# Kernel tuning notes

Hardware: AMD Instinct MI355X
Metric: run time of the kernel (lower is better)

## Reference

```python
import jax, jax.numpy as jnp
import numpy as np
import math

# Hardcoded model constants (from source globals)
N_LAYERS = 4
MAX_SEQ_LEN = 34
VOCAB_SIZE = 14
TOK_DIM = 3
POS_DIM = 3
D_MODEL = 6
HEAD_DIM = 3
N_POS = 10
MAX_DIGITS = 10
ANSWER_LEN = 11
X_START, PLUS_POS, Y_START, EQ_POS, Z_START, EOS_POS = 0, 10, 11, 21, 22, 33
PLUS_TOKEN, EQUALS_TOKEN, EOS_TOKEN, PAD_TOKEN = 10, 11, 12, 13
BATCH = 16384


def _spiral(i, p):
    return (math.cos(2 * math.pi * i / p), math.sin(2 * math.pi * i / p), i / max(p - 1, 1))


def _build_pos_enc():
    pe = np.zeros((MAX_SEQ_LEN, POS_DIM), np.float32)
    for i in range(MAX_DIGITS):
        pe[X_START + i] = _spiral(i, N_POS)
    for i in range(MAX_DIGITS):
        pe[Y_START + i] = _spiral(i, N_POS)
    for i in range(min(ANSWER_LEN, N_POS)):
        pe[Z_START + i] = _spiral(i, N_POS)
    pe[Z_START + 10] = [0.0, 0.0, 1.5]
    pe[PLUS_POS] = [2.0, 0.0, -1.0]
    pe[EQ_POS] = [0.0, 2.0, -1.0]
    pe[EOS_POS] = [-2.0, 0.0, -1.0]
    return jnp.asarray(pe)


def _build_tok_emb():
    emb = np.zeros((VOCAB_SIZE, TOK_DIM), np.float32)
    for d in range(10):
        emb[d] = _spiral(d, 10)
    emb[PLUS_TOKEN] = [2.0, 0.0, -1.0]
    emb[EQUALS_TOKEN] = [0.0, 2.0, -1.0]
    emb[EOS_TOKEN] = [-2.0, 0.0, -1.0]
    emb[PAD_TOKEN] = [0.0, -2.0, -1.0]
    return jnp.asarray(emb)


def _xavier(key, shape):
    fan_out, fan_in = shape[-2], shape[-1]
    bound = math.sqrt(6.0 / (fan_in + fan_out))
    return jax.random.uniform(key, shape, jnp.float32, -bound, bound)


def setup_inputs() -> dict:
    key = jax.random.key(0)
    ks = jax.random.split(key, 10)
    L = N_LAYERS
    return {
        "idx": jax.random.randint(ks[0], (BATCH, MAX_SEQ_LEN), 0, VOCAB_SIZE),
        "tok_emb": _build_tok_emb(),
        "pos_enc": _build_pos_enc(),
        "ln_w": jnp.ones((L, D_MODEL), jnp.float32),
        "ln_b": jnp.zeros((L, D_MODEL), jnp.float32),
        "q1w": _xavier(ks[1], (L, HEAD_DIM, TOK_DIM)),
        "k1w": _xavier(ks[2], (L, HEAD_DIM, TOK_DIM)),
        "v1w": _xavier(ks[3], (L, HEAD_DIM, TOK_DIM)),
        "q2w": _xavier(ks[4], (L, HEAD_DIM, POS_DIM)),
        "k2w": _xavier(ks[5], (L, HEAD_DIM, POS_DIM)),
        "v2w": _xavier(ks[6], (L, HEAD_DIM, POS_DIM)),
        "out_w": _xavier(ks[7], (L, D_MODEL, 2 * HEAD_DIM)),
        "lnf_w": jnp.ones((D_MODEL,), jnp.float32),
        "lnf_b": jnp.zeros((D_MODEL,), jnp.float32),
        "head_w": _xavier(ks[8], (VOCAB_SIZE, D_MODEL)),
    }


def _layernorm(x, w, b, eps=1e-5):
    m = jnp.mean(x, -1, keepdims=True)
    v = jnp.mean(jnp.square(x - m), -1, keepdims=True)
    return (x - m) * jax.lax.rsqrt(v + eps) * w + b


def _attend(q, k, v, mask):
    # q,k,v: [B,T,HEAD_DIM]; mask: [T,T] bool lower-triangular
    s = jnp.einsum('bqd,bkd->bqk', q, k) / math.sqrt(HEAD_DIM)
    s = jnp.where(mask, s, jnp.finfo(s.dtype).min)
    return jnp.einsum('bqk,bkd->bqd', jax.nn.softmax(s, axis=-1), v)


def reference(idx, tok_emb, pos_enc, ln_w, ln_b, q1w, k1w, v1w, q2w, k2w, v2w, out_w, lnf_w, lnf_b, head_w):
    B, T = idx.shape
    tok = tok_emb[idx]                                   # [B,T,3]
    pos = jnp.broadcast_to(pos_enc[:T], (B, T, POS_DIM))  # [B,T,3]
    x = jnp.concatenate([tok, pos], axis=-1)             # [B,T,6]
    mask = jnp.tril(jnp.ones((T, T), bool))
    for l in range(N_LAYERS):
        h = _layernorm(x, ln_w[l], ln_b[l])
        ht, hp = h[..., :TOK_DIM], h[..., TOK_DIM:]
        o1 = _attend(ht @ q1w[l].T, ht @ k1w[l].T, ht @ v1w[l].T, mask)
        o2 = _attend(hp @ q2w[l].T, hp @ k2w[l].T, hp @ v2w[l].T, mask)
        x = x + jnp.concatenate([o1, o2], axis=-1) @ out_w[l].T
    x = _layernorm(x, lnf_w, lnf_b)
    return x @ head_w.T                                  # [B,T,VOCAB]
```

## Files before the change

### kernel.cpp

```cpp
#include <hip/hip_runtime.h>
#include <math.h>

#define N_LAYERS 4
#define SEQ      34
#define BATCH_N  16384
#define NE       16
#define NSLOT    8
#define NT       5
#define VOCAB    14
#define QSCALE   0.8329806647638704f

typedef float f32x2 __attribute__((ext_vector_type(2)));

static __device__ __forceinline__ f32x2 mk2(float a, float b) {
    f32x2 r; r.x = a; r.y = b; return r;
}

__global__ __launch_bounds__(128) void addtrans_kernel(
    const int*   __restrict__ idx,
    const float* __restrict__ tok_emb,
    const float* __restrict__ pos_enc,
    const float* __restrict__ ln_w,
    const float* __restrict__ ln_b,
    const float* __restrict__ q1w,
    const float* __restrict__ k1w,
    const float* __restrict__ v1w,
    const float* __restrict__ q2w,
    const float* __restrict__ k2w,
    const float* __restrict__ v2w,
    const float* __restrict__ out_w,
    const float* __restrict__ lnf_w,
    const float* __restrict__ lnf_b,
    const float* __restrict__ head_w,
    float* __restrict__ out)
{
    __shared__ float4 kvs[3 * SEQ + 1][NE];

    const int x = threadIdx.x & (NE - 1);
    const int y = threadIdx.x >> 4;
    const int b = (int)blockIdx.x * NE + x;

    int tp[NT];
    tp[0] = (y < 2) ? (32 + y) : (24 + y);
    tp[1] = y;
    tp[2] = 8 + y;
    tp[3] = 16 + y;
    tp[4] = (y < 2) ? (24 + y) : -1;
    const int jmax = tp[0];

    float xs[NT][6];
    #pragma unroll
    for (int k = 0; k < NT; ++k) {
        const int t = tp[k];
        if (t >= 0) {
            const int tok = idx[(size_t)b * SEQ + t];
            xs[k][0] = tok_emb[tok * 3 + 0];
            xs[k][1] = tok_emb[tok * 3 + 1];
            xs[k][2] = tok_emb[tok * 3 + 2];
            xs[k][3] = pos_enc[t * 3 + 0];
            xs[k][4] = pos_enc[t * 3 + 1];
            xs[k][5] = pos_enc[t * 3 + 2];
        }
    }

    f32x2 qp[NT][3];

    for (int l = 0; l < N_LAYERS; ++l) {
        __syncthreads();

        #pragma unroll
        for (int k = 0; k < NT; ++k) {
            const int t = tp[k];
            if (t >= 0) {
                float h[6];
                {
                    const float* v = xs[k];
                    float m = (v[0]+v[1]+v[2]+v[3]+v[4]+v[5]) * (1.0f/6.0f);
                    float var = 0.f;
                    #pragma unroll
                    for (int i = 0; i < 6; ++i) { float d = v[i]-m; var += d*d; }
                    var *= (1.0f/6.0f);
                    float r = rsqrtf(var + 1e-5f);
                    #pragma unroll
                    for (int i = 0; i < 6; ++i)
                        h[i] = (v[i]-m) * r * ln_w[l*6+i] + ln_b[l*6+i];
                }
                float kk[6], vv[6];
                #pragma unroll
                for (int i = 0; i < 3; ++i) {
                    const int w = l*9 + i*3;
                    float q1 = (q1w[w]*h[0] + q1w[w+1]*h[1] + q1w[w+2]*h[2]) * QSCALE;
                    float q2 = (q2w[w]*h[3] + q2w[w+1]*h[4] + q2w[w+2]*h[5]) * QSCALE;
                    qp[k][i] = mk2(q1, q2);
                    kk[i]    =  k1w[w]*h[0] + k1w[w+1]*h[1] + k1w[w+2]*h[2];
                    vv[i]    =  v1w[w]*h[0] + v1w[w+1]*h[1] + v1w[w+2]*h[2];
                    kk[3+i]  =  k2w[w]*h[3] + k2w[w+1]*h[4] + k2w[w+2]*h[5];
                    vv[3+i]  =  v2w[w]*h[3] + v2w[w+1]*h[4] + v2w[w+2]*h[5];
                }
                kvs[0*SEQ + t][x] = make_float4(kk[0], kk[3], kk[1], kk[4]);
                kvs[1*SEQ + t][x] = make_float4(kk[2], kk[5], vv[0], vv[3]);
                kvs[2*SEQ + t][x] = make_float4(vv[1], vv[4], vv[2], vv[5]);
            }
        }
        __syncthreads();

        f32x2 ls[NT], acc[NT][3];
        #pragma unroll
        for (int k = 0; k < NT; ++k) {
            ls[k] = mk2(0.f, 0.f);
            acc[k][0] = acc[k][1] = acc[k][2] = mk2(0.f, 0.f);
        }
        float4 c0 = kvs[0][x], c1 = kvs[SEQ][x], c2 = kvs[2*SEQ][x];
        #pragma unroll 2
        for (int j = 0; j <= jmax; ++j) {
            float4 n0 = kvs[j + 1][x];
            float4 n1 = kvs[SEQ + j + 1][x];
            float4 n2 = kvs[2*SEQ + j + 1][x];
            f32x2 kp0 = mk2(c0.x, c0.y), kp1 = mk2(c0.z, c0.w), kp2 = mk2(c1.x, c1.y);
            f32x2 vp0 = mk2(c1.z, c1.w), vp1 = mk2(c2.x, c2.y), vp2 = mk2(c2.z, c2.w);
            #pragma unroll
            for (int k = 0; k < NT; ++k) {
                if (k == 0 || j <= tp[k]) {
                    f32x2 s = qp[k][0]*kp0 + qp[k][1]*kp1 + qp[k][2]*kp2;
                    f32x2 p = mk2(__builtin_amdgcn_exp2f(s.x),
                                  __builtin_amdgcn_exp2f(s.y));
                    ls[k] += p;
                    acc[k][0] += p*vp0; acc[k][1] += p*vp1; acc[k][2] += p*vp2;
                }
            }
            c0 = n0; c1 = n1; c2 = n2;
        }

        #pragma unroll
        for (int k = 0; k < NT; ++k) {
            if (tp[k] >= 0) {
                const float i1 = __builtin_amdgcn_rcpf(ls[k].x);
                const float i2 = __builtin_amdgcn_rcpf(ls[k].y);
                float o[6] = { acc[k][0].x*i1, acc[k][1].x*i1, acc[k][2].x*i1,
                               acc[k][0].y*i2, acc[k][1].y*i2, acc[k][2].y*i2 };
                #pragma unroll
                for (int i = 0; i < 6; ++i) {
                    const int w = l*36 + i*6;
                    xs[k][i] += out_w[w+0]*o[0] + out_w[w+1]*o[1] + out_w[w+2]*o[2]
                              + out_w[w+3]*o[3] + out_w[w+4]*o[4] + out_w[w+5]*o[5];
                }
            }
        }
    }

    #pragma unroll
    for (int k = 0; k < NT; ++k) {
        const int t = tp[k];
        if (t >= 0) {
            float hf[6];
            {
                const float* v = xs[k];
                float m = (v[0]+v[1]+v[2]+v[3]+v[4]+v[5]) * (1.0f/6.0f);
                float var = 0.f;
                #pragma unroll
                for (int i = 0; i < 6; ++i) { float d = v[i]-m; var += d*d; }
                var *= (1.0f/6.0f);
                float r = rsqrtf(var + 1e-5f);
                #pragma unroll
                for (int i = 0; i < 6; ++i)
                    hf[i] = (v[i]-m) * r * lnf_w[i] + lnf_b[i];
            }
            float lg[VOCAB];
            #pragma unroll
            for (int c = 0; c < VOCAB; ++c) {
                const int w = c*6;
                lg[c] = head_w[w+0]*hf[0] + head_w[w+1]*hf[1] + head_w[w+2]*hf[2]
                      + head_w[w+3]*hf[3] + head_w[w+4]*hf[4] + head_w[w+5]*hf[5];
            }
            float2* op = (float2*)(out + ((size_t)b * SEQ + t) * VOCAB);
            #pragma unroll
            for (int c = 0; c < 7; ++c)
                op[c] = make_float2(lg[2*c], lg[2*c+1]);
        }
    }
}

extern "C" void kernel_launch(void* const* d_in, const int* in_sizes, int n_in,
                              void* d_out, int out_size, void* d_ws, size_t ws_size,
                              hipStream_t stream) {
    const int*   idx     = (const int*)  d_in[0];
    const float* tok_emb = (const float*)d_in[1];
    const float* pos_enc = (const float*)d_in[2];
    const float* ln_w    = (const float*)d_in[3];
    const float* ln_b    = (const float*)d_in[4];
    const float* q1w     = (const float*)d_in[5];
    const float* k1w     = (const float*)d_in[6];
    const float* v1w     = (const float*)d_in[7];
    const float* q2w     = (const float*)d_in[8];
    const float* k2w     = (const float*)d_in[9];
    const float* v2w     = (const float*)d_in[10];
    const float* out_w   = (const float*)d_in[11];
    const float* lnf_w   = (const float*)d_in[12];
    const float* lnf_b   = (const float*)d_in[13];
    const float* head_w  = (const float*)d_in[14];
    float* out = (float*)d_out;

    const int grid = BATCH_N / NE;
    addtrans_kernel<<<grid, NE * NSLOT, 0, stream>>>(
        idx, tok_emb, pos_enc, ln_w, ln_b,
        q1w, k1w, v1w, q2w, k2w, v2w,
        out_w, lnf_w, lnf_b, head_w, out);
}
```

Measured before the change: 139.4 us.

## Stage logits in shared memory for coalesced float4 stores and pack math into f32x2

The final logits are written into a shared-memory staging buffer laid out per block, then copied to global memory with fully coalesced float4 stores instead of strided per-thread float2 stores. The K/V shared layout becomes interleaved per position, [t][3][NE], instead of three separate planes. The Q/K/V projections, output projection and head matmul are rewritten with packed f32x2 arithmetic. This enlarges shared memory per block, which may lower occupancy, and adds an extra barrier and copy pass.

```diff
diff --git a/kernel.cpp b/kernel.cpp
--- a/kernel.cpp
+++ b/kernel.cpp
@@ -15,6 +15,8 @@
 static __device__ __forceinline__ f32x2 mk2(float a, float b) {
     f32x2 r; r.x = a; r.y = b; return r;
 }
+
+#define SM_BYTES (NE * SEQ * VOCAB * 4)
 
 __global__ __launch_bounds__(128) void addtrans_kernel(
     const int*   __restrict__ idx,
@@ -34,7 +36,8 @@
     const float* __restrict__ head_w,
     float* __restrict__ out)
 {
-    __shared__ float4 kvs[3 * SEQ + 1][NE];
+    __shared__ __align__(16) char smraw[SM_BYTES];
+    float4 (*kvs)[3][NE] = (float4 (*)[3][NE])smraw;
 
     const int x = threadIdx.x & (NE - 1);
     const int y = threadIdx.x >> 4;
@@ -85,21 +88,27 @@
                     for (int i = 0; i < 6; ++i)
                         h[i] = (v[i]-m) * r * ln_w[l*6+i] + ln_b[l*6+i];
                 }
-                float kk[6], vv[6];
+                f32x2 hp0 = mk2(h[0], h[3]);
+                f32x2 hp1 = mk2(h[1], h[4]);
+                f32x2 hp2 = mk2(h[2], h[5]);
+                f32x2 kkp[3], vvp[3];
                 #pragma unroll
                 for (int i = 0; i < 3; ++i) {
                     const int w = l*9 + i*3;
-                    float q1 = (q1w[w]*h[0] + q1w[w+1]*h[1] + q1w[w+2]*h[2]) * QSCALE;
-                    float q2 = (q2w[w]*h[3] + q2w[w+1]*h[4] + q2w[w+2]*h[5]) * QSCALE;
-                    qp[k][i] = mk2(q1, q2);
-                    kk[i]    =  k1w[w]*h[0] + k1w[w+1]*h[1] + k1w[w+2]*h[2];
-                    vv[i]    =  v1w[w]*h[0] + v1w[w+1]*h[1] + v1w[w+2]*h[2];
-                    kk[3+i]  =  k2w[w]*h[3] + k2w[w+1]*h[4] + k2w[w+2]*h[5];
-                    vv[3+i]  =  v2w[w]*h[3] + v2w[w+1]*h[4] + v2w[w+2]*h[5];
-                }
-                kvs[0*SEQ + t][x] = make_float4(kk[0], kk[3], kk[1], kk[4]);
-                kvs[1*SEQ + t][x] = make_float4(kk[2], kk[5], vv[0], vv[3]);
-                kvs[2*SEQ + t][x] = make_float4(vv[1], vv[4], vv[2], vv[5]);
+                    f32x2 q = mk2(q1w[w  ], q2w[w  ]) * hp0
+                            + mk2(q1w[w+1], q2w[w+1]) * hp1
+                            + mk2(q1w[w+2], q2w[w+2]) * hp2;
+                    qp[k][i] = q * QSCALE;
+                    kkp[i]   = mk2(k1w[w  ], k2w[w  ]) * hp0
+                             + mk2(k1w[w+1], k2w[w+1]) * hp1
+                             + mk2(k1w[w+2], k2w[w+2]) * hp2;
+                    vvp[i]   = mk2(v1w[w  ], v2w[w  ]) * hp0
+                             + mk2(v1w[w+1], v2w[w+1]) * hp1
+                             + mk2(v1w[w+2], v2w[w+2]) * hp2;
+                }
+                kvs[t][0][x] = make_float4(kkp[0].x, kkp[0].y, kkp[1].x, kkp[1].y);
+                kvs[t][1][x] = make_float4(kkp[2].x, kkp[2].y, vvp[0].x, vvp[0].y);
+                kvs[t][2][x] = make_float4(vvp[1].x, vvp[1].y, vvp[2].x, vvp[2].y);
             }
         }
         __syncthreads();
@@ -110,12 +119,14 @@
             ls[k] = mk2(0.f, 0.f);
             acc[k][0] = acc[k][1] = acc[k][2] = mk2(0.f, 0.f);
         }
-        float4 c0 = kvs[0][x], c1 = kvs[SEQ][x], c2 = kvs[2*SEQ][x];
+        const float4* r0 = &kvs[0][0][x];
+        float4 c0 = r0[0*NE], c1 = r0[1*NE], c2 = r0[2*NE];
         #pragma unroll 2
         for (int j = 0; j <= jmax; ++j) {
-            float4 n0 = kvs[j + 1][x];
-            float4 n1 = kvs[SEQ + j + 1][x];
-            float4 n2 = kvs[2*SEQ + j + 1][x];
+            const float4* rn = &kvs[j + 1][0][x];
+            float4 n0 = rn[0*NE];
+            float4 n1 = rn[1*NE];
+            float4 n2 = rn[2*NE];
             f32x2 kp0 = mk2(c0.x, c0.y), kp1 = mk2(c0.z, c0.w), kp2 = mk2(c1.x, c1.y);
             f32x2 vp0 = mk2(c1.z, c1.w), vp1 = mk2(c2.x, c2.y), vp2 = mk2(c2.z, c2.w);
             #pragma unroll
@@ -134,20 +145,25 @@
         #pragma unroll
         for (int k = 0; k < NT; ++k) {
             if (tp[k] >= 0) {
-                const float i1 = __builtin_amdgcn_rcpf(ls[k].x);
-                const float i2 = __builtin_amdgcn_rcpf(ls[k].y);
-                float o[6] = { acc[k][0].x*i1, acc[k][1].x*i1, acc[k][2].x*i1,
-                               acc[k][0].y*i2, acc[k][1].y*i2, acc[k][2].y*i2 };
+                const f32x2 inv = mk2(__builtin_amdgcn_rcpf(ls[k].x),
+                                      __builtin_amdgcn_rcpf(ls[k].y));
+                f32x2 op0 = acc[k][0] * inv;
+                f32x2 op1 = acc[k][1] * inv;
+                f32x2 op2 = acc[k][2] * inv;
                 #pragma unroll
                 for (int i = 0; i < 6; ++i) {
                     const int w = l*36 + i*6;
-                    xs[k][i] += out_w[w+0]*o[0] + out_w[w+1]*o[1] + out_w[w+2]*o[2]
-                              + out_w[w+3]*o[3] + out_w[w+4]*o[4] + out_w[w+5]*o[5];
-                }
-            }
-        }
-    }
-
+                    f32x2 t2 = mk2(out_w[w+0], out_w[w+3]) * op0
+                             + mk2(out_w[w+1], out_w[w+4]) * op1
+                             + mk2(out_w[w+2], out_w[w+5]) * op2;
+                    xs[k][i] += t2.x + t2.y;
+                }
+            }
+        }
+    }
+
+    __syncthreads();
+    f32x2* st2 = (f32x2*)smraw;
     #pragma unroll
     for (int k = 0; k < NT; ++k) {
         const int t = tp[k];
@@ -165,18 +181,27 @@
                 for (int i = 0; i < 6; ++i)
                     hf[i] = (v[i]-m) * r * lnf_w[i] + lnf_b[i];
             }
-            float lg[VOCAB];
             #pragma unroll
-            for (int c = 0; c < VOCAB; ++c) {
-                const int w = c*6;
-                lg[c] = head_w[w+0]*hf[0] + head_w[w+1]*hf[1] + head_w[w+2]*hf[2]
-                      + head_w[w+3]*hf[3] + head_w[w+4]*hf[4] + head_w[w+5]*hf[5];
-            }
-            float2* op = (float2*)(out + ((size_t)b * SEQ + t) * VOCAB);
-            #pragma unroll
-            for (int c = 0; c < 7; ++c)
-                op[c] = make_float2(lg[2*c], lg[2*c+1]);
-        }
+            for (int c = 0; c < 7; ++c) {
+                const int w0 = (2*c) * 6, w1 = (2*c + 1) * 6;
+                f32x2 lg = mk2(head_w[w0+0], head_w[w1+0]) * hf[0]
+                         + mk2(head_w[w0+1], head_w[w1+1]) * hf[1]
+                         + mk2(head_w[w0+2], head_w[w1+2]) * hf[2]
+                         + mk2(head_w[w0+3], head_w[w1+3]) * hf[3]
+                         + mk2(head_w[w0+4], head_w[w1+4]) * hf[4]
+                         + mk2(head_w[w0+5], head_w[w1+5]) * hf[5];
+                st2[x*238 + t*7 + c] = lg;
+            }
+        }
+    }
+    __syncthreads();
+
+    {
+        const float4* st4 = (const float4*)smraw;
+        float4* o4 = (float4*)(out + (size_t)blockIdx.x * (NE * SEQ * VOCAB));
+        #pragma unroll
+        for (int i = threadIdx.x; i < (NE * SEQ * VOCAB) / 4; i += NE * NSLOT)
+            o4[i] = st4[i];
     }
 }
 
```

Result: slower. 148.7 us (+6.7%).

## Assign contiguous query-row blocks per thread slot and specialize attention loop by row count

Applied to the files above, without the earlier changes.

Replaces the strided assignment of sequence positions to the 8 thread slots with contiguous runs of 5, 3 or 4 rows, chosen so causal-attention work is roughly balanced across slots. Because each slot's rows are adjacent, its key loop length (jmax) covers little wasted work for the lower rows. The attention loop is instantiated separately for 5-row and 4-row slots so the smaller variant uses fewer registers and skips the unused row. The cost is code duplication and the wave-level divergence between y<4 and y>=4 branches, although each wave of 64 threads holds 4 slots with the same y class.

```diff
diff --git a/kernel.cpp b/kernel.cpp
--- a/kernel.cpp
+++ b/kernel.cpp
@@ -40,12 +40,15 @@
     const int y = threadIdx.x >> 4;
     const int b = (int)blockIdx.x * NE + x;
 
+    int base, nrows;
+    if (y < 4) { base = 5 * y;                                nrows = 5; }
+    else { const int z = y - 4;
+           base  = (z < 2) ? (20 + 3 * z) : (26 + 4 * (z - 2));
+           nrows = (z < 2) ? 3 : 4; }
     int tp[NT];
-    tp[0] = (y < 2) ? (32 + y) : (24 + y);
-    tp[1] = y;
-    tp[2] = 8 + y;
-    tp[3] = 16 + y;
-    tp[4] = (y < 2) ? (24 + y) : -1;
+    #pragma unroll
+    for (int k = 0; k < NT; ++k)
+        tp[k] = (k < nrows) ? (base + nrows - 1 - k) : -1;
     const int jmax = tp[0];
 
     float xs[NT][6];
@@ -64,6 +67,51 @@
     }
 
     f32x2 qp[NT][3];
+
+    #define ATTN_EPI(NTK) \
+    { \
+        f32x2 ls[NTK], acc[NTK][3]; \
+        _Pragma("unroll") \
+        for (int k = 0; k < NTK; ++k) { \
+            ls[k] = mk2(0.f, 0.f); \
+            acc[k][0] = acc[k][1] = acc[k][2] = mk2(0.f, 0.f); \
+        } \
+        float4 c0 = kvs[0][x], c1 = kvs[SEQ][x], c2 = kvs[2*SEQ][x]; \
+        _Pragma("unroll 2") \
+        for (int j = 0; j <= jmax; ++j) { \
+            float4 n0 = kvs[j + 1][x]; \
+            float4 n1 = kvs[SEQ + j + 1][x]; \
+            float4 n2 = kvs[2*SEQ + j + 1][x]; \
+            f32x2 kp0 = mk2(c0.x, c0.y), kp1 = mk2(c0.z, c0.w), kp2 = mk2(c1.x, c1.y); \
+            f32x2 vp0 = mk2(c1.z, c1.w), vp1 = mk2(c2.x, c2.y), vp2 = mk2(c2.z, c2.w); \
+            _Pragma("unroll") \
+            for (int k = 0; k < NTK; ++k) { \
+                if (k == 0 || j <= tp[k]) {    \
+                    f32x2 s = qp[k][0]*kp0 + qp[k][1]*kp1 + qp[k][2]*kp2; \
+                    f32x2 p = mk2(__builtin_amdgcn_exp2f(s.x), \
+                                  __builtin_amdgcn_exp2f(s.y)); \
+                    ls[k] += p; \
+                    acc[k][0] += p*vp0; acc[k][1] += p*vp1; acc[k][2] += p*vp2; \
+                } \
+            } \
+            c0 = n0; c1 = n1; c2 = n2; \
+        } \
+        _Pragma("unroll") \
+        for (int k = 0; k < NTK; ++k) { \
+            if (tp[k] >= 0) { \
+                const float i1 = __builtin_amdgcn_rcpf(ls[k].x); \
+                const float i2 = __builtin_amdgcn_rcpf(ls[k].y); \
+                float o[6] = { acc[k][0].x*i1, acc[k][1].x*i1, acc[k][2].x*i1, \
+                               acc[k][0].y*i2, acc[k][1].y*i2, acc[k][2].y*i2 }; \
+                _Pragma("unroll") \
+                for (int i = 0; i < 6; ++i) { \
+                    const int w = l*36 + i*6; \
+                    xs[k][i] += out_w[w+0]*o[0] + out_w[w+1]*o[1] + out_w[w+2]*o[2] \
+                              + out_w[w+3]*o[3] + out_w[w+4]*o[4] + out_w[w+5]*o[5]; \
+                } \
+            } \
+        } \
+    }
 
     for (int l = 0; l < N_LAYERS; ++l) {
         __syncthreads();
@@ -104,49 +152,9 @@
         }
         __syncthreads();
 
-        f32x2 ls[NT], acc[NT][3];
-        #pragma unroll
-        for (int k = 0; k < NT; ++k) {
-            ls[k] = mk2(0.f, 0.f);
-            acc[k][0] = acc[k][1] = acc[k][2] = mk2(0.f, 0.f);
-        }
-        float4 c0 = kvs[0][x], c1 = kvs[SEQ][x], c2 = kvs[2*SEQ][x];
-        #pragma unroll 2
-        for (int j = 0; j <= jmax; ++j) {
-            float4 n0 = kvs[j + 1][x];
-            float4 n1 = kvs[SEQ + j + 1][x];
-            float4 n2 = kvs[2*SEQ + j + 1][x];
-            f32x2 kp0 = mk2(c0.x, c0.y), kp1 = mk2(c0.z, c0.w), kp2 = mk2(c1.x, c1.y);
-            f32x2 vp0 = mk2(c1.z, c1.w), vp1 = mk2(c2.x, c2.y), vp2 = mk2(c2.z, c2.w);
-            #pragma unroll
-            for (int k = 0; k < NT; ++k) {
-                if (k == 0 || j <= tp[k]) {
-                    f32x2 s = qp[k][0]*kp0 + qp[k][1]*kp1 + qp[k][2]*kp2;
-                    f32x2 p = mk2(__builtin_amdgcn_exp2f(s.x),
-                                  __builtin_amdgcn_exp2f(s.y));
-                    ls[k] += p;
-                    acc[k][0] += p*vp0; acc[k][1] += p*vp1; acc[k][2] += p*vp2;
-                }
-            }
-            c0 = n0; c1 = n1; c2 = n2;
-        }
-
-        #pragma unroll
-        for (int k = 0; k < NT; ++k) {
-            if (tp[k] >= 0) {
-                const float i1 = __builtin_amdgcn_rcpf(ls[k].x);
-                const float i2 = __builtin_amdgcn_rcpf(ls[k].y);
-                float o[6] = { acc[k][0].x*i1, acc[k][1].x*i1, acc[k][2].x*i1,
-                               acc[k][0].y*i2, acc[k][1].y*i2, acc[k][2].y*i2 };
-                #pragma unroll
-                for (int i = 0; i < 6; ++i) {
-                    const int w = l*36 + i*6;
-                    xs[k][i] += out_w[w+0]*o[0] + out_w[w+1]*o[1] + out_w[w+2]*o[2]
-                              + out_w[w+3]*o[3] + out_w[w+4]*o[4] + out_w[w+5]*o[5];
-                }
-            }
-        }
-    }
+        if (y < 4) { ATTN_EPI(5) } else { ATTN_EPI(4) }
+    }
+    #undef ATTN_EPI
 
     #pragma unroll
     for (int k = 0; k < NT; ++k) {
```

Measured after the change: 141.3 us. No clear change (+1.4%).

## Split attention key range across two half-waves and merge partial sums via shuffles

Applied to the files above, without the earlier changes.

Doubles the block to 256 threads. Each pair of 16-lane halves now splits the key loop at position 17, with each half owning a subset of query positions for layernorm, projection and output. Queries are exchanged, and the partial softmax denominators and accumulators are combined with cross-lane xor shuffles. The shared buffer is also padded to NE+1 to change the bank mapping. The goal is to shorten the serial per-thread attention loop and raise parallelism, at the cost of extra shuffles, duplicated idle work for non-owned rows, and more threads per block.

```diff
diff --git a/kernel.cpp b/kernel.cpp
--- a/kernel.cpp
+++ b/kernel.cpp
@@ -8,6 +8,7 @@
 #define NSLOT    8
 #define NT       5
 #define VOCAB    14
+#define SPLIT    17
 #define QSCALE   0.8329806647638704f
 
 typedef float f32x2 __attribute__((ext_vector_type(2)));
@@ -16,7 +17,7 @@
     f32x2 r; r.x = a; r.y = b; return r;
 }
 
-__global__ __launch_bounds__(128) void addtrans_kernel(
+__global__ __launch_bounds__(256) void addtrans_kernel(
     const int*   __restrict__ idx,
     const float* __restrict__ tok_emb,
     const float* __restrict__ pos_enc,
@@ -34,10 +35,11 @@
     const float* __restrict__ head_w,
     float* __restrict__ out)
 {
-    __shared__ float4 kvs[3 * SEQ + 1][NE];
+    __shared__ float4 kvs[3 * SEQ + 1][NE + 1];
 
     const int x = threadIdx.x & (NE - 1);
-    const int y = threadIdx.x >> 4;
+    const int h = (threadIdx.x >> 4) & 1;
+    const int y = threadIdx.x >> 5;
     const int b = (int)blockIdx.x * NE + x;
 
     int tp[NT];
@@ -48,11 +50,15 @@
     tp[4] = (y < 2) ? (24 + y) : -1;
     const int jmax = tp[0];
 
+    bool own[NT];
+    own[0] = (h == 1); own[1] = (h == 0); own[2] = (h == 0);
+    own[3] = (h == 1); own[4] = (h == 1);
+
     float xs[NT][6];
     #pragma unroll
     for (int k = 0; k < NT; ++k) {
         const int t = tp[k];
-        if (t >= 0) {
+        if (t >= 0 && own[k]) {
             const int tok = idx[(size_t)b * SEQ + t];
             xs[k][0] = tok_emb[tok * 3 + 0];
             xs[k][1] = tok_emb[tok * 3 + 1];
@@ -69,10 +75,14 @@
         __syncthreads();
 
         #pragma unroll
+        for (int k = 0; k < NT; ++k)
+            qp[k][0] = qp[k][1] = qp[k][2] = mk2(0.f, 0.f);
+
+        #pragma unroll
         for (int k = 0; k < NT; ++k) {
             const int t = tp[k];
-            if (t >= 0) {
-                float h[6];
+            if (t >= 0 && own[k]) {
+                float hh[6];
                 {
                     const float* v = xs[k];
                     float m = (v[0]+v[1]+v[2]+v[3]+v[4]+v[5]) * (1.0f/6.0f);
@@ -83,25 +93,35 @@
                     float r = rsqrtf(var + 1e-5f);
                     #pragma unroll
                     for (int i = 0; i < 6; ++i)
-                        h[i] = (v[i]-m) * r * ln_w[l*6+i] + ln_b[l*6+i];
+                        hh[i] = (v[i]-m) * r * ln_w[l*6+i] + ln_b[l*6+i];
                 }
                 float kk[6], vv[6];
                 #pragma unroll
                 for (int i = 0; i < 3; ++i) {
                     const int w = l*9 + i*3;
-                    float q1 = (q1w[w]*h[0] + q1w[w+1]*h[1] + q1w[w+2]*h[2]) * QSCALE;
-                    float q2 = (q2w[w]*h[3] + q2w[w+1]*h[4] + q2w[w+2]*h[5]) * QSCALE;
+                    float q1 = (q1w[w]*hh[0] + q1w[w+1]*hh[1] + q1w[w+2]*hh[2]) * QSCALE;
+                    float q2 = (q2w[w]*hh[3] + q2w[w+1]*hh[4] + q2w[w+2]*hh[5]) * QSCALE;
                     qp[k][i] = mk2(q1, q2);
-                    kk[i]    =  k1w[w]*h[0] + k1w[w+1]*h[1] + k1w[w+2]*h[2];
-                    vv[i]    =  v1w[w]*h[0] + v1w[w+1]*h[1] + v1w[w+2]*h[2];
-                    kk[3+i]  =  k2w[w]*h[3] + k2w[w+1]*h[4] + k2w[w+2]*h[5];
-                    vv[3+i]  =  v2w[w]*h[3] + v2w[w+1]*h[4] + v2w[w+2]*h[5];
+                    kk[i]    =  k1w[w]*hh[0] + k1w[w+1]*hh[1] + k1w[w+2]*hh[2];
+                    vv[i]    =  v1w[w]*hh[0] + v1w[w+1]*hh[1] + v1w[w+2]*hh[2];
+                    kk[3+i]  =  k2w[w]*hh[3] + k2w[w+1]*hh[4] + k2w[w+2]*hh[5];
+                    vv[3+i]  =  v2w[w]*hh[3] + v2w[w+1]*hh[4] + v2w[w+2]*hh[5];
                 }
                 kvs[0*SEQ + t][x] = make_float4(kk[0], kk[3], kk[1], kk[4]);
                 kvs[1*SEQ + t][x] = make_float4(kk[2], kk[5], vv[0], vv[3]);
                 kvs[2*SEQ + t][x] = make_float4(vv[1], vv[4], vv[2], vv[5]);
             }
         }
+
+        #pragma unroll
+        for (int k = 0; k < NT; ++k) {
+            #pragma unroll
+            for (int i = 0; i < 3; ++i) {
+                float ax = __shfl_xor(qp[k][i].x, 16, 64);
+                float ay = __shfl_xor(qp[k][i].y, 16, 64);
+                if (!own[k]) qp[k][i] = mk2(ax, ay);
+            }
+        }
         __syncthreads();
 
         f32x2 ls[NT], acc[NT][3];
@@ -110,9 +130,11 @@
             ls[k] = mk2(0.f, 0.f);
             acc[k][0] = acc[k][1] = acc[k][2] = mk2(0.f, 0.f);
         }
-        float4 c0 = kvs[0][x], c1 = kvs[SEQ][x], c2 = kvs[2*SEQ][x];
+        const int jb = h ? SPLIT : 0;
+        float4 c0 = kvs[jb][x], c1 = kvs[SEQ + jb][x], c2 = kvs[2*SEQ + jb][x];
         #pragma unroll 2
-        for (int j = 0; j <= jmax; ++j) {
+        for (int jj = 0; jj < SPLIT; ++jj) {
+            const int j = jb + jj;
             float4 n0 = kvs[j + 1][x];
             float4 n1 = kvs[SEQ + j + 1][x];
             float4 n2 = kvs[2*SEQ + j + 1][x];
@@ -120,7 +142,7 @@
             f32x2 vp0 = mk2(c1.z, c1.w), vp1 = mk2(c2.x, c2.y), vp2 = mk2(c2.z, c2.w);
             #pragma unroll
             for (int k = 0; k < NT; ++k) {
-                if (k == 0 || j <= tp[k]) {
+                if (j <= tp[k]) {
                     f32x2 s = qp[k][0]*kp0 + qp[k][1]*kp1 + qp[k][2]*kp2;
                     f32x2 p = mk2(__builtin_amdgcn_exp2f(s.x),
                                   __builtin_amdgcn_exp2f(s.y));
@@ -133,7 +155,20 @@
 
         #pragma unroll
         for (int k = 0; k < NT; ++k) {
-            if (tp[k] >= 0) {
+            if (k == 0 || k >= 3) {
+                ls[k].x += __shfl_xor(ls[k].x, 16, 64);
+                ls[k].y += __shfl_xor(ls[k].y, 16, 64);
+                #pragma unroll
+                for (int i = 0; i < 3; ++i) {
+                    acc[k][i].x += __shfl_xor(acc[k][i].x, 16, 64);
+                    acc[k][i].y += __shfl_xor(acc[k][i].y, 16, 64);
+                }
+            }
+        }
+
+        #pragma unroll
+        for (int k = 0; k < NT; ++k) {
+            if (tp[k] >= 0 && own[k]) {
                 const float i1 = __builtin_amdgcn_rcpf(ls[k].x);
                 const float i2 = __builtin_amdgcn_rcpf(ls[k].y);
                 float o[6] = { acc[k][0].x*i1, acc[k][1].x*i1, acc[k][2].x*i1,
@@ -151,7 +186,7 @@
     #pragma unroll
     for (int k = 0; k < NT; ++k) {
         const int t = tp[k];
-        if (t >= 0) {
+        if (t >= 0 && own[k]) {
             float hf[6];
             {
                 const float* v = xs[k];
@@ -201,7 +236,7 @@
     float* out = (float*)d_out;
 
     const int grid = BATCH_N / NE;
-    addtrans_kernel<<<grid, NE * NSLOT, 0, stream>>>(
+    addtrans_kernel<<<grid, 256, 0, stream>>>(
         idx, tok_emb, pos_enc, ln_w, ln_b,
         q1w, k1w, v1w, q2w, k2w, v2w,
         out_w, lnf_w, lnf_b, head_w, out);
```

Result: slower. 183.6 us (+31.8%).
